# Kernel optimization log

Measured on AMD Instinct MI355X. Metric: run time of the kernel, lower is better.

## Reference

```python
import jax, jax.numpy as jnp
import numpy as np

WINDOW = 5
HALF = WINDOW // 2


def setup_inputs() -> dict:
    key = jax.random.key(0)
    ks = jax.random.split(key, 6)
    C, H_f, W_f = 128, 640, 640
    N = 20000
    Wc = W_f // 4  # coarse grid width (fine_ratio = stride//2 = 4)
    mk0 = jax.random.uniform(ks[0], (N, 2), jnp.float32, 0.0, Wc - 1.0)
    mk1 = jax.random.uniform(ks[1], (N, 2), jnp.float32, 0.0, Wc - 1.0)
    f0 = jax.random.normal(ks[2], (1, C, H_f, W_f), jnp.float32)
    f1 = jax.random.normal(ks[3], (1, C, H_f, W_f), jnp.float32)
    pw = jax.random.normal(ks[4], (C, C), jnp.float32) / np.sqrt(C).astype(np.float32)
    pb = jax.random.normal(ks[5], (C,), jnp.float32) * 0.01
    return {"mkpts0_coarse": mk0, "mkpts1_coarse": mk1,
            "feat_fine0": f0, "feat_fine1": f1,
            "proj_w": pw, "proj_b": pb, "stride": 8}


def reference(mkpts0_coarse, mkpts1_coarse, feat_fine0, feat_fine1, proj_w, proj_b, stride):
    # 1x1 conv projection (batch dim is always indexed at 0 in the original)
    f0 = jnp.einsum('oc,chw->ohw', proj_w, feat_fine0[0]) + proj_b[:, None, None]
    f1 = jnp.einsum('oc,chw->ohw', proj_w, feat_fine1[0]) + proj_b[:, None, None]
    C, H_f, W_f = f0.shape
    fine_ratio = stride // 2
    c0 = (mkpts0_coarse * fine_ratio).astype(jnp.int32)
    c1 = (mkpts1_coarse * fine_ratio).astype(jnp.int32)
    cx0, cy0 = c0[:, 0], c0[:, 1]
    cx1, cy1 = c1[:, 0], c1[:, 1]
    valid = ((cx0 >= HALF) & (cx0 + HALF < W_f) & (cy0 >= HALF) & (cy0 + HALF < H_f)
             & (cx1 >= HALF) & (cx1 + HALF < W_f) & (cy1 >= HALF) & (cy1 + HALF < H_f))
    # clamp centers so gathers stay in-bounds; invalid matches masked afterwards
    cx0c = jnp.clip(cx0, HALF, W_f - 1 - HALF)
    cy0c = jnp.clip(cy0, HALF, H_f - 1 - HALF)
    cx1c = jnp.clip(cx1, HALF, W_f - 1 - HALF)
    cy1c = jnp.clip(cy1, HALF, H_f - 1 - HALF)
    center_feat = f0[:, cy0c, cx0c].T  # (N, C): center pixel of each 5x5 window in image 0
    d = jnp.arange(-HALF, HALF + 1)
    yidx = cy1c[:, None, None] + d[None, :, None]  # (N, W, 1)
    xidx = cx1c[:, None, None] + d[None, None, :]  # (N, 1, W)
    patch1 = f1[:, yidx, xidx]  # (C, N, W, W) window crops from image 1
    corr = jnp.einsum('nc,cnhw->nhw', center_feat, patch1)  # (N, W, W)
    corr_soft = jax.nn.softmax(corr.reshape(-1, WINDOW * WINDOW), axis=1)
    corr_soft = corr_soft.reshape(-1, WINDOW, WINDOW)
    gy, gx = jnp.meshgrid(jnp.arange(WINDOW, dtype=f0.dtype) - HALF,
                          jnp.arange(WINDOW, dtype=f0.dtype) - HALF, indexing='ij')
    off_x = (corr_soft * gx).sum(axis=(1, 2))
    off_y = (corr_soft * gy).sum(axis=(1, 2))
    scale = stride // fine_ratio  # = 2 for default stride
    off = jnp.stack([off_x, off_y], axis=1) * scale  # (N, 2)
    off = jnp.where(valid[:, None], off, 0.0)
    pts0 = mkpts0_coarse * stride + stride // 2
    pts1 = mkpts1_coarse * stride + stride // 2 + off
    return pts0, pts1
```

## Files before the change

### kernel.cpp

```cpp
#include <hip/hip_runtime.h>
#include <math.h>

#define CCH 128
#define WIN 5
#define HALFW 2
#define TP 131

__device__ __forceinline__ unsigned short f2bf(float f) {
    unsigned int b = __float_as_uint(f);
    b += 0x7FFFu + ((b >> 16) & 1u);
    return (unsigned short)(b >> 16);
}
__device__ __forceinline__ float bf2f(unsigned short u) {
    return __uint_as_float(((unsigned int)u) << 16);
}

__global__ __launch_bounds__(CCH) void fr_precompute(const float* __restrict__ pw,
                                                     const float* __restrict__ pb,
                                                     float* __restrict__ Mv) {
    const int c = blockIdx.x;
    const int t = threadIdx.x;
    float s = 0.f;
    if (c < CCH) {
        #pragma unroll 4
        for (int o = 0; o < CCH; ++o) s = fmaf(pw[o * CCH + c], pw[o * CCH + t], s);
        Mv[c * CCH + t] = s;
    } else {
        #pragma unroll 4
        for (int o = 0; o < CCH; ++o) s = fmaf(pb[o], pw[o * CCH + t], s);
        Mv[CCH * CCH + t] = s;
    }
}

__global__ __launch_bounds__(256) void fr_transpose_bf16(const float* __restrict__ feat1,
                                                         unsigned short* __restrict__ ft,
                                                         long HW) {
    __shared__ float lds[64 * TP];
    const long pix0 = (long)blockIdx.x * 64;
    const int tid = threadIdx.x;

    {
        const int s16 = tid & 15;
        const int grp = tid >> 4;
        #pragma unroll
        for (int it = 0; it < 8; ++it) {
            const int c = grp + it * 16;
            const float4 v = *(const float4*)&feat1[(long)c * HW + pix0 + s16 * 4];
            lds[(s16 * 4 + 0) * TP + c] = v.x;
            lds[(s16 * 4 + 1) * TP + c] = v.y;
            lds[(s16 * 4 + 2) * TP + c] = v.z;
            lds[(s16 * 4 + 3) * TP + c] = v.w;
        }
    }
    __syncthreads();

    {
        const int cq = tid & 31;
        const int pq = tid >> 5;
        #pragma unroll
        for (int it = 0; it < 8; ++it) {
            const int pp = pq + it * 8;
            const float* row = &lds[pp * TP + cq * 4];
            ushort4 o;
            o.x = f2bf(row[0]); o.y = f2bf(row[1]);
            o.z = f2bf(row[2]); o.w = f2bf(row[3]);
            *(ushort4*)&ft[((pix0 + pp) * CCH) + cq * 4] = o;
        }
    }
}

__global__ __launch_bounds__(256) void fr_refine2(
    const float* __restrict__ mk0, const float* __restrict__ mk1,
    const float* __restrict__ feat0, const unsigned short* __restrict__ ft,
    const float* __restrict__ Mv, const int* __restrict__ stride_p,
    float* __restrict__ out, int N, int H, int W) {

    const int tid = threadIdx.x;
    const int pt  = tid >> 5;
    const int sub = tid & 31;
    const int n   = blockIdx.x * 8 + pt;
    const int nn  = (n < N) ? n : 0;
    const long HW = (long)H * W;

    const int stride = *stride_p;
    const int fine_ratio = stride >> 1;
    const float frf = (float)fine_ratio;
    const float scale = (float)(stride / fine_ratio);
    const float half_s = (float)(stride >> 1);

    const float2 m0 = *(const float2*)&mk0[2 * nn];
    const float2 m1 = *(const float2*)&mk1[2 * nn];

    const int cx0 = (int)(m0.x * frf), cy0 = (int)(m0.y * frf);
    const int cx1 = (int)(m1.x * frf), cy1 = (int)(m1.y * frf);

    const bool valid =
        (cx0 >= HALFW) && (cx0 + HALFW < W) && (cy0 >= HALFW) && (cy0 + HALFW < H) &&
        (cx1 >= HALFW) && (cx1 + HALFW < W) && (cy1 >= HALFW) && (cy1 + HALFW < H);

    const int cx0c = min(max(cx0, HALFW), W - 1 - HALFW);
    const int cy0c = min(max(cy0, HALFW), H - 1 - HALFW);
    const int cx1c = min(max(cx1, HALFW), W - 1 - HALFW);
    const int cy1c = min(max(cy1, HALFW), H - 1 - HALFW);

    __shared__ float sh_x0[8][CCH];

    {
        const long off0 = (long)cy0c * W + cx0c;
        float4 x0v;
        x0v.x = feat0[(long)(4 * sub + 0) * HW + off0];
        x0v.y = feat0[(long)(4 * sub + 1) * HW + off0];
        x0v.z = feat0[(long)(4 * sub + 2) * HW + off0];
        x0v.w = feat0[(long)(4 * sub + 3) * HW + off0];
        *(float4*)&sh_x0[pt][4 * sub] = x0v;
    }
    __syncthreads();

    float4 g = *(const float4*)&Mv[CCH * CCH + 4 * sub];
    {
        const float4* shx = (const float4*)sh_x0[pt];
        #pragma unroll 8
        for (int c4 = 0; c4 < 32; ++c4) {
            const float4 xv = shx[c4];
            const float4 r0 = *(const float4*)&Mv[(c4 * 4 + 0) * CCH + 4 * sub];
            const float4 r1 = *(const float4*)&Mv[(c4 * 4 + 1) * CCH + 4 * sub];
            const float4 r2 = *(const float4*)&Mv[(c4 * 4 + 2) * CCH + 4 * sub];
            const float4 r3 = *(const float4*)&Mv[(c4 * 4 + 3) * CCH + 4 * sub];
            g.x = fmaf(r0.x, xv.x, g.x); g.y = fmaf(r0.y, xv.x, g.y);
            g.z = fmaf(r0.z, xv.x, g.z); g.w = fmaf(r0.w, xv.x, g.w);
            g.x = fmaf(r1.x, xv.y, g.x); g.y = fmaf(r1.y, xv.y, g.y);
            g.z = fmaf(r1.z, xv.y, g.z); g.w = fmaf(r1.w, xv.y, g.w);
            g.x = fmaf(r2.x, xv.z, g.x); g.y = fmaf(r2.y, xv.z, g.y);
            g.z = fmaf(r2.z, xv.z, g.z); g.w = fmaf(r2.w, xv.z, g.w);
            g.x = fmaf(r3.x, xv.w, g.x); g.y = fmaf(r3.y, xv.w, g.y);
            g.z = fmaf(r3.z, xv.w, g.z); g.w = fmaf(r3.w, xv.w, g.w);
        }
    }

    ushort4 u[25];
    {
        const long pbase = (long)(cy1c - HALFW) * W + (cx1c - HALFW);
        #pragma unroll
        for (int dy = 0; dy < WIN; ++dy) {
            #pragma unroll
            for (int dx = 0; dx < WIN; ++dx) {
                const long pix = pbase + (long)dy * W + dx;
                u[dy * WIN + dx] = *(const ushort4*)&ft[pix * CCH + 4 * sub];
            }
        }
    }

    float corr[25];
    #pragma unroll
    for (int j = 0; j < 25; ++j) {
        float v = g.x * bf2f(u[j].x) + g.y * bf2f(u[j].y) +
                  g.z * bf2f(u[j].z) + g.w * bf2f(u[j].w);
        v += __shfl_down(v, 16, 32);
        v += __shfl_down(v, 8, 32);
        v += __shfl_down(v, 4, 32);
        v += __shfl_down(v, 2, 32);
        v += __shfl_down(v, 1, 32);
        corr[j] = v;
    }

    if (sub == 0 && n < N) {
        float mx = -1e30f;
        #pragma unroll
        for (int j = 0; j < 25; ++j) mx = fmaxf(mx, corr[j]);
        float sum = 0.f;
        #pragma unroll
        for (int j = 0; j < 25; ++j) {
            const float e = __expf(corr[j] - mx);
            corr[j] = e;
            sum += e;
        }
        const float inv = 1.f / sum;
        float ox = 0.f, oy = 0.f;
        #pragma unroll
        for (int j = 0; j < 25; ++j) {
            const float w = corr[j] * inv;
            ox += w * (float)(j % WIN - HALFW);
            oy += w * (float)(j / WIN - HALFW);
        }
        if (!valid) { ox = 0.f; oy = 0.f; }
        const float sf = (float)stride;
        float2 p0, p1;
        p0.x = m0.x * sf + half_s;
        p0.y = m0.y * sf + half_s;
        p1.x = m1.x * sf + half_s + ox * scale;
        p1.y = m1.y * sf + half_s + oy * scale;
        *(float2*)&out[2 * n] = p0;
        *(float2*)&out[2 * N + 2 * n] = p1;
    }
}

__global__ __launch_bounds__(CCH) void fr_refine_fb(
    const float* __restrict__ mk0, const float* __restrict__ mk1,
    const float* __restrict__ feat0, const float* __restrict__ feat1,
    const float* __restrict__ Mv, const int* __restrict__ stride_p,
    float* __restrict__ out, int N, int H, int W) {

    const int n = blockIdx.x;
    const int t = threadIdx.x;
    const long HW = (long)H * W;

    const int stride = *stride_p;
    const int fine_ratio = stride >> 1;
    const float frf = (float)fine_ratio;
    const float scale = (float)(stride / fine_ratio);
    const float half_s = (float)(stride >> 1);

    const float m0x = mk0[2 * n], m0y = mk0[2 * n + 1];
    const float m1x = mk1[2 * n], m1y = mk1[2 * n + 1];

    const int cx0 = (int)(m0x * frf), cy0 = (int)(m0y * frf);
    const int cx1 = (int)(m1x * frf), cy1 = (int)(m1y * frf);

    const bool valid =
        (cx0 >= HALFW) && (cx0 + HALFW < W) && (cy0 >= HALFW) && (cy0 + HALFW < H) &&
        (cx1 >= HALFW) && (cx1 + HALFW < W) && (cy1 >= HALFW) && (cy1 + HALFW < H);

    const int cx0c = min(max(cx0, HALFW), W - 1 - HALFW);
    const int cy0c = min(max(cy0, HALFW), H - 1 - HALFW);
    const int cx1c = min(max(cx1, HALFW), W - 1 - HALFW);
    const int cy1c = min(max(cy1, HALFW), H - 1 - HALFW);

    __shared__ float sh_x0[CCH];
    __shared__ float red[2 * 25];

    sh_x0[t] = feat0[(long)t * HW + (long)cy0c * W + cx0c];
    __syncthreads();

    float g = Mv[CCH * CCH + t];
    #pragma unroll 8
    for (int c = 0; c < CCH; ++c) g = fmaf(Mv[c * CCH + t], sh_x0[c], g);

    const float* f1b = feat1 + (long)t * HW + (long)(cy1c - HALFW) * W + (cx1c - HALFW);
    float prod[25];
    #pragma unroll
    for (int dy = 0; dy < WIN; ++dy)
        #pragma unroll
        for (int dx = 0; dx < WIN; ++dx)
            prod[dy * WIN + dx] = g * f1b[(long)dy * W + dx];

    const int lane = t & 63;
    const int wv = t >> 6;
    #pragma unroll
    for (int j = 0; j < 25; ++j) {
        float v = prod[j];
        v += __shfl_down(v, 32);
        v += __shfl_down(v, 16);
        v += __shfl_down(v, 8);
        v += __shfl_down(v, 4);
        v += __shfl_down(v, 2);
        v += __shfl_down(v, 1);
        if (lane == 0) red[wv * 25 + j] = v;
    }
    __syncthreads();

    if (t == 0) {
        float corr[25];
        float mx = -1e30f;
        #pragma unroll
        for (int j = 0; j < 25; ++j) { corr[j] = red[j] + red[25 + j]; mx = fmaxf(mx, corr[j]); }
        float sum = 0.f;
        #pragma unroll
        for (int j = 0; j < 25; ++j) { const float e = __expf(corr[j] - mx); corr[j] = e; sum += e; }
        const float inv = 1.f / sum;
        float ox = 0.f, oy = 0.f;
        #pragma unroll
        for (int j = 0; j < 25; ++j) {
            const float w = corr[j] * inv;
            ox += w * (float)(j % WIN - HALFW);
            oy += w * (float)(j / WIN - HALFW);
        }
        if (!valid) { ox = 0.f; oy = 0.f; }
        const float sf = (float)stride;
        out[2 * N + 2 * n]     = m1x * sf + half_s + ox * scale;
        out[2 * N + 2 * n + 1] = m1y * sf + half_s + oy * scale;
        out[2 * n]     = m0x * sf + half_s;
        out[2 * n + 1] = m0y * sf + half_s;
    }
}

extern "C" void kernel_launch(void* const* d_in, const int* in_sizes, int n_in,
                              void* d_out, int out_size, void* d_ws, size_t ws_size,
                              hipStream_t stream) {
    const float* mk0 = (const float*)d_in[0];
    const float* mk1 = (const float*)d_in[1];
    const float* f0  = (const float*)d_in[2];
    const float* f1  = (const float*)d_in[3];
    const float* pw  = (const float*)d_in[4];
    const float* pb  = (const float*)d_in[5];
    const int*   sp  = (const int*)d_in[6];

    const int N = in_sizes[0] / 2;
    const long HW = (long)in_sizes[2] / CCH;
    const int Wf = (int)(sqrt((double)HW) + 0.5);
    const int Hf = (int)(HW / Wf);

    const size_t mv_bytes = (size_t)(CCH * CCH + CCH) * sizeof(float);
    const size_t ft_bytes = (size_t)HW * CCH * sizeof(unsigned short);
    const bool use_ft = (ws_size >= mv_bytes + ft_bytes);

    float* Mv = (float*)d_ws;
    unsigned short* ft = (unsigned short*)((char*)d_ws + mv_bytes);

    fr_precompute<<<CCH + 1, CCH, 0, stream>>>(pw, pb, Mv);

    if (use_ft) {
        fr_transpose_bf16<<<(int)(HW / 64), 256, 0, stream>>>(f1, ft, HW);
        fr_refine2<<<(N + 7) / 8, 256, 0, stream>>>(mk0, mk1, f0, ft, Mv, sp,
                                                    (float*)d_out, N, Hf, Wf);
    } else {
        fr_refine_fb<<<N, CCH, 0, stream>>>(mk0, mk1, f0, f1, Mv, sp,
                                            (float*)d_out, N, Hf, Wf);
    }
}
```

Baseline: 495.6 us.

## Fuse feat1 transpose with per-match GEMV into one heterogeneous launch

```diff
diff --git a/kernel.cpp b/kernel.cpp
--- a/kernel.cpp
+++ b/kernel.cpp
@@ -5,6 +5,7 @@
 #define WIN 5
 #define HALFW 2
 #define TP 131
+#define TRANS_PIX 64
 
 __device__ __forceinline__ unsigned short f2bf(float f) {
     unsigned int b = __float_as_uint(f);
@@ -32,93 +33,79 @@
     }
 }
 
-__global__ __launch_bounds__(256) void fr_transpose_bf16(const float* __restrict__ feat1,
-                                                         unsigned short* __restrict__ ft,
-                                                         long HW) {
-    __shared__ float lds[64 * TP];
-    const long pix0 = (long)blockIdx.x * 64;
+__global__ __launch_bounds__(256) void fr_trans_gemv(
+    const float* __restrict__ feat1, unsigned short* __restrict__ ft,
+    const float* __restrict__ mk0, const float* __restrict__ feat0,
+    const float* __restrict__ Mv, float* __restrict__ G,
+    const int* __restrict__ stride_p,
+    long HW, int N, int H, int W, int TB, int GB) {
+
+    __shared__ float smem[TRANS_PIX * TP];
+    const int b = blockIdx.x;
+    const int total = TB + GB;
+    const long tb_lo = ((long)b * TB) / total;
+    const long tb_hi = ((long)(b + 1) * TB) / total;
+    const bool is_trans = (tb_hi > tb_lo);
     const int tid = threadIdx.x;
 
-    {
-        const int s16 = tid & 15;
-        const int grp = tid >> 4;
-        #pragma unroll
-        for (int it = 0; it < 8; ++it) {
-            const int c = grp + it * 16;
-            const float4 v = *(const float4*)&feat1[(long)c * HW + pix0 + s16 * 4];
-            lds[(s16 * 4 + 0) * TP + c] = v.x;
-            lds[(s16 * 4 + 1) * TP + c] = v.y;
-            lds[(s16 * 4 + 2) * TP + c] = v.z;
-            lds[(s16 * 4 + 3) * TP + c] = v.w;
-        }
-    }
-    __syncthreads();
-
-    {
-        const int cq = tid & 31;
-        const int pq = tid >> 5;
-        #pragma unroll
-        for (int it = 0; it < 8; ++it) {
-            const int pp = pq + it * 8;
-            const float* row = &lds[pp * TP + cq * 4];
-            ushort4 o;
-            o.x = f2bf(row[0]); o.y = f2bf(row[1]);
-            o.z = f2bf(row[2]); o.w = f2bf(row[3]);
-            *(ushort4*)&ft[((pix0 + pp) * CCH) + cq * 4] = o;
-        }
-    }
-}
-
-__global__ __launch_bounds__(256) void fr_refine2(
-    const float* __restrict__ mk0, const float* __restrict__ mk1,
-    const float* __restrict__ feat0, const unsigned short* __restrict__ ft,
-    const float* __restrict__ Mv, const int* __restrict__ stride_p,
-    float* __restrict__ out, int N, int H, int W) {
-
-    const int tid = threadIdx.x;
-    const int pt  = tid >> 5;
-    const int sub = tid & 31;
-    const int n   = blockIdx.x * 8 + pt;
-    const int nn  = (n < N) ? n : 0;
-    const long HW = (long)H * W;
-
-    const int stride = *stride_p;
-    const int fine_ratio = stride >> 1;
-    const float frf = (float)fine_ratio;
-    const float scale = (float)(stride / fine_ratio);
-    const float half_s = (float)(stride >> 1);
-
-    const float2 m0 = *(const float2*)&mk0[2 * nn];
-    const float2 m1 = *(const float2*)&mk1[2 * nn];
-
-    const int cx0 = (int)(m0.x * frf), cy0 = (int)(m0.y * frf);
-    const int cx1 = (int)(m1.x * frf), cy1 = (int)(m1.y * frf);
-
-    const bool valid =
-        (cx0 >= HALFW) && (cx0 + HALFW < W) && (cy0 >= HALFW) && (cy0 + HALFW < H) &&
-        (cx1 >= HALFW) && (cx1 + HALFW < W) && (cy1 >= HALFW) && (cy1 + HALFW < H);
-
-    const int cx0c = min(max(cx0, HALFW), W - 1 - HALFW);
-    const int cy0c = min(max(cy0, HALFW), H - 1 - HALFW);
-    const int cx1c = min(max(cx1, HALFW), W - 1 - HALFW);
-    const int cy1c = min(max(cy1, HALFW), H - 1 - HALFW);
-
-    __shared__ float sh_x0[8][CCH];
-
-    {
-        const long off0 = (long)cy0c * W + cx0c;
-        float4 x0v;
-        x0v.x = feat0[(long)(4 * sub + 0) * HW + off0];
-        x0v.y = feat0[(long)(4 * sub + 1) * HW + off0];
-        x0v.z = feat0[(long)(4 * sub + 2) * HW + off0];
-        x0v.w = feat0[(long)(4 * sub + 3) * HW + off0];
-        *(float4*)&sh_x0[pt][4 * sub] = x0v;
-    }
-    __syncthreads();
-
-    float4 g = *(const float4*)&Mv[CCH * CCH + 4 * sub];
-    {
-        const float4* shx = (const float4*)sh_x0[pt];
+    if (is_trans) {
+        const long pix0 = tb_lo * TRANS_PIX;
+        {
+            const int s16 = tid & 15;
+            const int grp = tid >> 4;
+            #pragma unroll
+            for (int it = 0; it < 8; ++it) {
+                const int c = grp + it * 16;
+                const float4 v = *(const float4*)&feat1[(long)c * HW + pix0 + s16 * 4];
+                smem[(s16 * 4 + 0) * TP + c] = v.x;
+                smem[(s16 * 4 + 1) * TP + c] = v.y;
+                smem[(s16 * 4 + 2) * TP + c] = v.z;
+                smem[(s16 * 4 + 3) * TP + c] = v.w;
+            }
+        }
+        __syncthreads();
+        {
+            const int cq = tid & 31;
+            const int pq = tid >> 5;
+            #pragma unroll
+            for (int it = 0; it < 8; ++it) {
+                const int pp = pq + it * 8;
+                const float* row = &smem[pp * TP + cq * 4];
+                ushort4 o;
+                o.x = f2bf(row[0]); o.y = f2bf(row[1]);
+                o.z = f2bf(row[2]); o.w = f2bf(row[3]);
+                *(ushort4*)&ft[((pix0 + pp) * CCH) + cq * 4] = o;
+            }
+        }
+    } else {
+        const int gb = b - (int)tb_lo;
+        const int pt  = tid >> 5;
+        const int sub = tid & 31;
+        const int n   = gb * 8 + pt;
+        const int nn  = (n < N) ? n : 0;
+
+        const int stride = *stride_p;
+        const float frf = (float)(stride >> 1);
+
+        const float2 m0 = *(const float2*)&mk0[2 * nn];
+        const int cx0 = (int)(m0.x * frf), cy0 = (int)(m0.y * frf);
+        const int cx0c = min(max(cx0, HALFW), W - 1 - HALFW);
+        const int cy0c = min(max(cy0, HALFW), H - 1 - HALFW);
+
+        float* sh_x0 = smem;
+        {
+            const long off0 = (long)cy0c * W + cx0c;
+            float4 x0v;
+            x0v.x = feat0[(long)(4 * sub + 0) * HW + off0];
+            x0v.y = feat0[(long)(4 * sub + 1) * HW + off0];
+            x0v.z = feat0[(long)(4 * sub + 2) * HW + off0];
+            x0v.w = feat0[(long)(4 * sub + 3) * HW + off0];
+            *(float4*)&sh_x0[pt * CCH + 4 * sub] = x0v;
+        }
+        __syncthreads();
+
+        float4 g = *(const float4*)&Mv[CCH * CCH + 4 * sub];
+        const float4* shx = (const float4*)&sh_x0[pt * CCH];
         #pragma unroll 8
         for (int c4 = 0; c4 < 32; ++c4) {
             const float4 xv = shx[c4];
@@ -135,7 +122,42 @@
             g.x = fmaf(r3.x, xv.w, g.x); g.y = fmaf(r3.y, xv.w, g.y);
             g.z = fmaf(r3.z, xv.w, g.z); g.w = fmaf(r3.w, xv.w, g.w);
         }
-    }
+        if (n < N) *(float4*)&G[(long)n * CCH + 4 * sub] = g;
+    }
+}
+
+__global__ __launch_bounds__(256) void fr_taps(
+    const float* __restrict__ mk0, const float* __restrict__ mk1,
+    const unsigned short* __restrict__ ft, const float* __restrict__ G,
+    const int* __restrict__ stride_p,
+    float* __restrict__ out, int N, int H, int W) {
+
+    const int tid = threadIdx.x;
+    const int pt  = tid >> 5;
+    const int sub = tid & 31;
+    const int n   = blockIdx.x * 8 + pt;
+    const int nn  = (n < N) ? n : 0;
+
+    const int stride = *stride_p;
+    const int fine_ratio = stride >> 1;
+    const float frf = (float)fine_ratio;
+    const float scale = (float)(stride / fine_ratio);
+    const float half_s = (float)(stride >> 1);
+
+    const float2 m0 = *(const float2*)&mk0[2 * nn];
+    const float2 m1 = *(const float2*)&mk1[2 * nn];
+
+    const int cx0 = (int)(m0.x * frf), cy0 = (int)(m0.y * frf);
+    const int cx1 = (int)(m1.x * frf), cy1 = (int)(m1.y * frf);
+
+    const bool valid =
+        (cx0 >= HALFW) && (cx0 + HALFW < W) && (cy0 >= HALFW) && (cy0 + HALFW < H) &&
+        (cx1 >= HALFW) && (cx1 + HALFW < W) && (cy1 >= HALFW) && (cy1 + HALFW < H);
+
+    const int cx1c = min(max(cx1, HALFW), W - 1 - HALFW);
+    const int cy1c = min(max(cy1, HALFW), H - 1 - HALFW);
+
+    const float4 g = *(const float4*)&G[(long)nn * CCH + 4 * sub];
 
     ushort4 u[25];
     {
@@ -300,18 +322,23 @@
     const int Hf = (int)(HW / Wf);
 
     const size_t mv_bytes = (size_t)(CCH * CCH + CCH) * sizeof(float);
+    const size_t g_bytes  = (size_t)N * CCH * sizeof(float);
     const size_t ft_bytes = (size_t)HW * CCH * sizeof(unsigned short);
-    const bool use_ft = (ws_size >= mv_bytes + ft_bytes);
+    const bool use_ft = (ws_size >= mv_bytes + g_bytes + ft_bytes);
 
     float* Mv = (float*)d_ws;
-    unsigned short* ft = (unsigned short*)((char*)d_ws + mv_bytes);
+    float* G  = (float*)((char*)d_ws + mv_bytes);
+    unsigned short* ft = (unsigned short*)((char*)d_ws + mv_bytes + g_bytes);
 
     fr_precompute<<<CCH + 1, CCH, 0, stream>>>(pw, pb, Mv);
 
     if (use_ft) {
-        fr_transpose_bf16<<<(int)(HW / 64), 256, 0, stream>>>(f1, ft, HW);
-        fr_refine2<<<(N + 7) / 8, 256, 0, stream>>>(mk0, mk1, f0, ft, Mv, sp,
-                                                    (float*)d_out, N, Hf, Wf);
+        const int TB = (int)(HW / TRANS_PIX);
+        const int GB = (N + 7) / 8;
+        fr_trans_gemv<<<TB + GB, 256, 0, stream>>>(f1, ft, mk0, f0, Mv, G, sp,
+                                                   HW, N, Hf, Wf, TB, GB);
+        fr_taps<<<(N + 7) / 8, 256, 0, stream>>>(mk0, mk1, ft, G, sp,
+                                                 (float*)d_out, N, Hf, Wf);
     } else {
         fr_refine_fb<<<N, CCH, 0, stream>>>(mk0, mk1, f0, f1, Mv, sp,
                                             (float*)d_out, N, Hf, Wf);
```

New measurement: 506.1 us. 1.02x slower.
